# Kernel tuning notes

Hardware: AMD Instinct MI355X
Metric: run time of the kernel (lower is better)

The kernel has to match this reference:

```python
import jax, jax.numpy as jnp
import numpy as np

K = 1.0        # Lorentz manifold curvature parameter
EPS = 1e-7     # arccosh argument clamp (geoopt float32 eps)


def projx(x):
    # Project onto the hyperboloid: x0 = sqrt(K + ||x_1:||^2)
    rest = x[..., 1:]
    x0 = jnp.sqrt(K + jnp.sum(rest * rest, axis=-1, keepdims=True))
    return jnp.concatenate([x0, rest], axis=-1)


def setup_inputs() -> dict:
    key = jax.random.key(0)
    k1, k2 = jax.random.split(key)
    B, C, D = 16384, 2048, 512
    x = jax.random.normal(k1, (B, D), dtype=jnp.float32)
    # ManifoldParameter: random_normal with std = 1/sqrt(n_dim)
    points = jax.random.normal(k2, (C, D), dtype=jnp.float32) * (1.0 / np.sqrt(D))
    return {"x": x, "points": points}


def reference(x, points):
    xp = projx(x)        # (B, D) on hyperboloid
    pp = projx(points)   # (C, D) on hyperboloid
    # Minkowski inner <x,p>_L = -x0*p0 + sum_{i>0} x_i p_i = x.p - 2*x0*p0
    # Computed as a GEMM plus a rank-1 correction (avoids (B,C,D) intermediate).
    inner = xp @ pp.T - 2.0 * jnp.outer(xp[:, 0], pp[:, 0])  # (B, C)
    d = jnp.sqrt(K) * jnp.arccosh(jnp.maximum(-inner / K, 1.0 + EPS))
    return -d  # (B, C) negative Riemannian distances (class logits)
```

## Files before the change

### kernel.cpp

```cpp
#include <hip/hip_runtime.h>
#include <hip/hip_bf16.h>
#include <stdint.h>

#define B_ROWS 16384
#define C_ROWS 2048
#define D_FULL 512
#define KP     512

#define BM 128
#define BN 128
#define BK 64

typedef __attribute__((ext_vector_type(8))) short bf16x8;
typedef __attribute__((ext_vector_type(4))) float f32x4;

typedef __attribute__((address_space(1))) void glb_void;
typedef __attribute__((address_space(3))) void lds_void;

__device__ __forceinline__ void gld16(const void* g, void* l) {
    __builtin_amdgcn_global_load_lds((glb_void*)(uintptr_t)g,
                                     (lds_void*)(uintptr_t)l, 16, 0, 0);
}

__global__ __launch_bounds__(256) void prep_kernel(
    const float* __restrict__ x, const float* __restrict__ pts,
    unsigned short* __restrict__ Abf, unsigned short* __restrict__ Bbf,
    float* __restrict__ xn, float* __restrict__ pn)
{
    int row = blockIdx.x;
    const float* src;
    unsigned short* dst;
    float* nrm;
    if (row < B_ROWS) {
        src = x + (size_t)row * D_FULL;
        dst = Abf + (size_t)row * KP;
        nrm = xn + row;
    } else {
        int r = row - B_ROWS;
        src = pts + (size_t)r * D_FULL;
        dst = Bbf + (size_t)r * KP;
        nrm = pn + r;
    }
    int t = threadIdx.x;
    float v0 = src[2 * t + 1];
    float v1 = (t < 255) ? src[2 * t + 2] : 0.0f;
    __hip_bfloat16 b0 = __float2bfloat16(v0);
    __hip_bfloat16 b1 = __float2bfloat16(v1);
    union { unsigned short u[2]; unsigned int w; } pack;
    pack.u[0] = *(unsigned short*)&b0;
    pack.u[1] = *(unsigned short*)&b1;
    *(unsigned int*)&dst[2 * t] = pack.w;
    float ss = v0 * v0 + v1 * v1;
    #pragma unroll
    for (int off = 32; off > 0; off >>= 1) ss += __shfl_down(ss, off);
    __shared__ float red[4];
    if ((t & 63) == 0) red[t >> 6] = ss;
    __syncthreads();
    if (t == 0) nrm[0] = sqrtf(1.0f + red[0] + red[1] + red[2] + red[3]);
}

__global__ __launch_bounds__(256, 2) void gemm_kernel(
    const unsigned short* __restrict__ A,
    const unsigned short* __restrict__ Bm,
    const float* __restrict__ xn, const float* __restrict__ pn,
    float* __restrict__ out)
{
    __shared__ unsigned short As[2][BM * BK];
    __shared__ unsigned short Bs[2][BN * BK];

    const int tid  = threadIdx.x;
    const int wave = tid >> 6;
    const int lane = tid & 63;
    const int wm   = wave >> 1;
    const int wn   = wave & 1;
    const int lrow = lane & 15;
    const int quad = lane >> 4;

    const int bm0 = blockIdx.x * BM;
    const int bn0 = blockIdx.y * BN;

    const int srow = wave * 32 + (lane >> 3);
    const int scol = (((lane & 7) ^ ((lane >> 3) & 7)) << 3);

    const unsigned short* gA = A  + (size_t)(bm0 + srow) * KP + scol;
    const unsigned short* gB = Bm + (size_t)(bn0 + srow) * KP + scol;

    f32x4 acc[4][4] = {};

    #pragma unroll
    for (int i = 0; i < 4; ++i) {
        gld16(gA + (size_t)(i * 8) * KP, &As[0][(wave * 32 + i * 8) * BK]);
        gld16(gB + (size_t)(i * 8) * KP, &Bs[0][(wave * 32 + i * 8) * BK]);
    }

    #pragma unroll 2
    for (int it = 0; it < KP / BK; ++it) {
        const int buf = it & 1;
        __syncthreads();
        if (it + 1 < KP / BK) {
            const int k1 = (it + 1) * BK;
            #pragma unroll
            for (int i = 0; i < 4; ++i) {
                gld16(gA + (size_t)(i * 8) * KP + k1, &As[buf ^ 1][(wave * 32 + i * 8) * BK]);
                gld16(gB + (size_t)(i * 8) * KP + k1, &Bs[buf ^ 1][(wave * 32 + i * 8) * BK]);
            }
        }
        #pragma unroll
        for (int kk = 0; kk < BK; kk += 32) {
            const int ch0 = kk >> 3;
            bf16x8 af[4], bfr[4];
            #pragma unroll
            for (int mi = 0; mi < 4; ++mi) {
                int r = wm * 64 + mi * 16 + lrow;
                af[mi] = *(const bf16x8*)&As[buf][r * BK + (((ch0 + quad) ^ (lrow & 7)) << 3)];
            }
            #pragma unroll
            for (int ni = 0; ni < 4; ++ni) {
                int r = wn * 64 + ni * 16 + lrow;
                bfr[ni] = *(const bf16x8*)&Bs[buf][r * BK + (((ch0 + quad) ^ (lrow & 7)) << 3)];
            }
            #pragma unroll
            for (int mi = 0; mi < 4; ++mi)
                #pragma unroll
                for (int ni = 0; ni < 4; ++ni)
                    acc[mi][ni] = __builtin_amdgcn_mfma_f32_16x16x32_bf16(
                        af[mi], bfr[ni], acc[mi][ni], 0, 0, 0);
        }
    }

    float pv[4];
    #pragma unroll
    for (int ni = 0; ni < 4; ++ni)
        pv[ni] = pn[bn0 + wn * 64 + ni * 16 + lrow];

    #pragma unroll
    for (int mi = 0; mi < 4; ++mi) {
        #pragma unroll
        for (int r = 0; r < 4; ++r) {
            int row = bm0 + wm * 64 + mi * 16 + quad * 4 + r;
            float xv = xn[row];
            size_t base = (size_t)row * C_ROWS + bn0 + wn * 64 + lrow;
            #pragma unroll
            for (int ni = 0; ni < 4; ++ni) {
                float z = fmaf(xv, pv[ni], -acc[mi][ni][r]);
                z = fmaxf(z, 1.0f + 1e-7f);
                out[base + ni * 16] = -__logf(z + __fsqrt_rn(z * z - 1.0f));
            }
        }
    }
}

extern "C" void kernel_launch(void* const* d_in, const int* in_sizes, int n_in,
                              void* d_out, int out_size, void* d_ws, size_t ws_size,
                              hipStream_t stream) {
    const float* x   = (const float*)d_in[0];
    const float* pts = (const float*)d_in[1];
    float* out = (float*)d_out;

    char* ws = (char*)d_ws;
    unsigned short* Abf = (unsigned short*)ws;
    unsigned short* Bbf = (unsigned short*)(ws + (size_t)B_ROWS * KP * 2);
    float* xn = (float*)(ws + (size_t)(B_ROWS + C_ROWS) * KP * 2);
    float* pn = (float*)((char*)xn + (size_t)B_ROWS * 4);
    (void)in_sizes; (void)n_in; (void)out_size; (void)ws_size;

    prep_kernel<<<B_ROWS + C_ROWS, 256, 0, stream>>>(x, pts, Abf, Bbf, xn, pn);

    dim3 grid(B_ROWS / BM, C_ROWS / BN);
    gemm_kernel<<<grid, 256, 0, stream>>>(Abf, Bbf, xn, pn, out);
}
```

Measured before the change: 196.1 us.

## Restructure GEMM into persistent strip blocks streaming full-K A chunks with B from global

Replaces the 2D tiled GEMM grid with 256 persistent blocks, each owning a 128-column strip of points and a range of 1024 rows of x. Each block streams 64-row full-K chunks of A into double-buffered LDS and reads B fragments directly from global (relying on cache), running the epilogue per chunk. The aim is to cut B reloads through LDS and launch overhead and to overlap the A prefetch with the epilogue. It risks low occupancy (one block per CU, large LDS), B fragment loads that hit global memory every k-step, and only 256 blocks to fill the device.

```diff
diff --git a/kernel.cpp b/kernel.cpp
--- a/kernel.cpp
+++ b/kernel.cpp
@@ -7,9 +7,10 @@
 #define D_FULL 512
 #define KP     512
 
-#define BM 128
-#define BN 128
-#define BK 64
+#define STRIPS  16
+#define MSPLIT  16
+#define CHUNK_M 64
+#define NCHUNK  16
 
 typedef __attribute__((ext_vector_type(8))) short bf16x8;
 typedef __attribute__((ext_vector_type(4))) float f32x4;
@@ -59,14 +60,13 @@
     if (t == 0) nrm[0] = sqrtf(1.0f + red[0] + red[1] + red[2] + red[3]);
 }
 
-__global__ __launch_bounds__(256, 2) void gemm_kernel(
+__global__ __launch_bounds__(256, 1) void gemm_kernel(
     const unsigned short* __restrict__ A,
     const unsigned short* __restrict__ Bm,
     const float* __restrict__ xn, const float* __restrict__ pn,
     float* __restrict__ out)
 {
-    __shared__ unsigned short As[2][BM * BK];
-    __shared__ unsigned short Bs[2][BN * BK];
+    __shared__ unsigned short As[2][CHUNK_M * KP];
 
     const int tid  = threadIdx.x;
     const int wave = tid >> 6;
@@ -76,75 +76,82 @@
     const int lrow = lane & 15;
     const int quad = lane >> 4;
 
-    const int bm0 = blockIdx.x * BM;
-    const int bn0 = blockIdx.y * BN;
+    const int m     = blockIdx.x & 15;
+    const int s     = blockIdx.x >> 4;
+    const int n0    = s * 128;
+    const int mBase = m * (CHUNK_M * NCHUNK);
 
-    const int srow = wave * 32 + (lane >> 3);
-    const int scol = (((lane & 7) ^ ((lane >> 3) & 7)) << 3);
+    const unsigned short* bPtr[4];
+    #pragma unroll
+    for (int nt = 0; nt < 4; ++nt)
+        bPtr[nt] = Bm + (size_t)(n0 + wn * 64 + nt * 16 + lrow) * KP + quad * 8;
 
-    const unsigned short* gA = A  + (size_t)(bm0 + srow) * KP + scol;
-    const unsigned short* gB = Bm + (size_t)(bn0 + srow) * KP + scol;
+    const int colEven = (lane ^ wave) << 3;
+    const int colOdd  = (lane ^ (wave + 4)) << 3;
 
-    f32x4 acc[4][4] = {};
+    const unsigned short* gA = A + (size_t)(mBase)*KP;
 
-    #pragma unroll
-    for (int i = 0; i < 4; ++i) {
-        gld16(gA + (size_t)(i * 8) * KP, &As[0][(wave * 32 + i * 8) * BK]);
-        gld16(gB + (size_t)(i * 8) * KP, &Bs[0][(wave * 32 + i * 8) * BK]);
-    }
-
-    #pragma unroll 2
-    for (int it = 0; it < KP / BK; ++it) {
-        const int buf = it & 1;
-        __syncthreads();
-        if (it + 1 < KP / BK) {
-            const int k1 = (it + 1) * BK;
-            #pragma unroll
-            for (int i = 0; i < 4; ++i) {
-                gld16(gA + (size_t)(i * 8) * KP + k1, &As[buf ^ 1][(wave * 32 + i * 8) * BK]);
-                gld16(gB + (size_t)(i * 8) * KP + k1, &Bs[buf ^ 1][(wave * 32 + i * 8) * BK]);
-            }
-        }
-        #pragma unroll
-        for (int kk = 0; kk < BK; kk += 32) {
-            const int ch0 = kk >> 3;
-            bf16x8 af[4], bfr[4];
-            #pragma unroll
-            for (int mi = 0; mi < 4; ++mi) {
-                int r = wm * 64 + mi * 16 + lrow;
-                af[mi] = *(const bf16x8*)&As[buf][r * BK + (((ch0 + quad) ^ (lrow & 7)) << 3)];
-            }
-            #pragma unroll
-            for (int ni = 0; ni < 4; ++ni) {
-                int r = wn * 64 + ni * 16 + lrow;
-                bfr[ni] = *(const bf16x8*)&Bs[buf][r * BK + (((ch0 + quad) ^ (lrow & 7)) << 3)];
-            }
-            #pragma unroll
-            for (int mi = 0; mi < 4; ++mi)
-                #pragma unroll
-                for (int ni = 0; ni < 4; ++ni)
-                    acc[mi][ni] = __builtin_amdgcn_mfma_f32_16x16x32_bf16(
-                        af[mi], bfr[ni], acc[mi][ni], 0, 0, 0);
-        }
-    }
+    const int sA = lrow & 7;
 
     float pv[4];
     #pragma unroll
-    for (int ni = 0; ni < 4; ++ni)
-        pv[ni] = pn[bn0 + wn * 64 + ni * 16 + lrow];
+    for (int nt = 0; nt < 4; ++nt)
+        pv[nt] = pn[n0 + wn * 64 + nt * 16 + lrow];
 
     #pragma unroll
-    for (int mi = 0; mi < 4; ++mi) {
+    for (int i = 0; i < 16; ++i) {
+        int r = i * 4 + wave;
+        gld16(gA + (size_t)r * KP + ((i & 1) ? colOdd : colEven), &As[0][r * KP]);
+    }
+
+    for (int ch = 0; ch < NCHUNK; ++ch) {
+        const int buf = ch & 1;
+        __syncthreads();
+
+        f32x4 acc[2][4] = {};
         #pragma unroll
-        for (int r = 0; r < 4; ++r) {
-            int row = bm0 + wm * 64 + mi * 16 + quad * 4 + r;
-            float xv = xn[row];
-            size_t base = (size_t)row * C_ROWS + bn0 + wn * 64 + lrow;
+        for (int ks = 0; ks < 16; ++ks) {
+            bf16x8 af[2], bfr[4];
             #pragma unroll
-            for (int ni = 0; ni < 4; ++ni) {
-                float z = fmaf(xv, pv[ni], -acc[mi][ni][r]);
-                z = fmaxf(z, 1.0f + 1e-7f);
-                out[base + ni * 16] = -__logf(z + __fsqrt_rn(z * z - 1.0f));
+            for (int mt = 0; mt < 2; ++mt) {
+                int rl = wm * 32 + mt * 16 + lrow;
+                int chunk = ((ks * 4 + quad) ^ sA);
+                af[mt] = *(const bf16x8*)&As[buf][rl * KP + (chunk << 3)];
+            }
+            #pragma unroll
+            for (int nt = 0; nt < 4; ++nt)
+                bfr[nt] = *(const bf16x8*)(bPtr[nt] + ks * 32);
+            #pragma unroll
+            for (int mt = 0; mt < 2; ++mt)
+                #pragma unroll
+                for (int nt = 0; nt < 4; ++nt)
+                    acc[mt][nt] = __builtin_amdgcn_mfma_f32_16x16x32_bf16(
+                        af[mt], bfr[nt], acc[mt][nt], 0, 0, 0);
+        }
+
+        if (ch + 1 < NCHUNK) {
+            const unsigned short* gAn = gA + (size_t)(ch + 1) * CHUNK_M * KP;
+            #pragma unroll
+            for (int i = 0; i < 16; ++i) {
+                int r = i * 4 + wave;
+                gld16(gAn + (size_t)r * KP + ((i & 1) ? colOdd : colEven),
+                      &As[buf ^ 1][r * KP]);
+            }
+        }
+
+        #pragma unroll
+        for (int mt = 0; mt < 2; ++mt) {
+            #pragma unroll
+            for (int r = 0; r < 4; ++r) {
+                int row = mBase + ch * CHUNK_M + wm * 32 + mt * 16 + quad * 4 + r;
+                float xv = xn[row];
+                size_t base = (size_t)row * C_ROWS + n0 + wn * 64 + lrow;
+                #pragma unroll
+                for (int nt = 0; nt < 4; ++nt) {
+                    float z = fmaf(xv, pv[nt], -acc[mt][nt][r]);
+                    z = fmaxf(z, 1.0f + 1e-7f);
+                    out[base + nt * 16] = -__logf(z + __fsqrt_rn(z * z - 1.0f));
+                }
             }
         }
     }
@@ -166,6 +173,5 @@
 
     prep_kernel<<<B_ROWS + C_ROWS, 256, 0, stream>>>(x, pts, Abf, Bbf, xn, pn);
 
-    dim3 grid(B_ROWS / BM, C_ROWS / BN);
-    gemm_kernel<<<grid, 256, 0, stream>>>(Abf, Bbf, xn, pn, out);
+    gemm_kernel<<<STRIPS * MSPLIT, 256, 0, stream>>>(Abf, Bbf, xn, pn, out);
 }
```

Measured after the change: 230.2 us. +17.4%, slower.

## Load B fragments directly from global into registers, bypassing LDS

Applied to the files above, without the earlier changes.

The B operand is no longer staged through shared memory. Each wave instead loads its bf16 B fragments straight from global memory into registers, with a one-step register prefetch. This halves LDS usage and removes the LDS reads for B, at the cost of more VGPRs and duplicate global loads across the waves that share B rows. The launch-bounds occupancy hint of 2 is also dropped, and the K loop is no longer unrolled by 2.

```diff
diff --git a/kernel.cpp b/kernel.cpp
--- a/kernel.cpp
+++ b/kernel.cpp
@@ -59,14 +59,13 @@
     if (t == 0) nrm[0] = sqrtf(1.0f + red[0] + red[1] + red[2] + red[3]);
 }
 
-__global__ __launch_bounds__(256, 2) void gemm_kernel(
+__global__ __launch_bounds__(256) void gemm_kernel(
     const unsigned short* __restrict__ A,
     const unsigned short* __restrict__ Bm,
     const float* __restrict__ xn, const float* __restrict__ pn,
     float* __restrict__ out)
 {
     __shared__ unsigned short As[2][BM * BK];
-    __shared__ unsigned short Bs[2][BN * BK];
 
     const int tid  = threadIdx.x;
     const int wave = tid >> 6;
@@ -81,51 +80,62 @@
 
     const int srow = wave * 32 + (lane >> 3);
     const int scol = (((lane & 7) ^ ((lane >> 3) & 7)) << 3);
+    const unsigned short* gA = A + (size_t)(bm0 + srow) * KP + scol;
 
-    const unsigned short* gA = A  + (size_t)(bm0 + srow) * KP + scol;
-    const unsigned short* gB = Bm + (size_t)(bn0 + srow) * KP + scol;
+    const unsigned short* bPtr[4];
+    #pragma unroll
+    for (int nt = 0; nt < 4; ++nt)
+        bPtr[nt] = Bm + (size_t)(bn0 + wn * 64 + nt * 16 + lrow) * KP + quad * 8;
 
     f32x4 acc[4][4] = {};
 
     #pragma unroll
-    for (int i = 0; i < 4; ++i) {
+    for (int i = 0; i < 4; ++i)
         gld16(gA + (size_t)(i * 8) * KP, &As[0][(wave * 32 + i * 8) * BK]);
-        gld16(gB + (size_t)(i * 8) * KP, &Bs[0][(wave * 32 + i * 8) * BK]);
-    }
 
-    #pragma unroll 2
+    bf16x8 bcur[2][4], bnxt[2][4];
+    #pragma unroll
+    for (int h = 0; h < 2; ++h)
+        #pragma unroll
+        for (int nt = 0; nt < 4; ++nt)
+            bcur[h][nt] = *(const bf16x8*)(bPtr[nt] + h * 32);
+
     for (int it = 0; it < KP / BK; ++it) {
         const int buf = it & 1;
+        const int k1 = (it + 1) * BK;
         __syncthreads();
         if (it + 1 < KP / BK) {
-            const int k1 = (it + 1) * BK;
             #pragma unroll
-            for (int i = 0; i < 4; ++i) {
-                gld16(gA + (size_t)(i * 8) * KP + k1, &As[buf ^ 1][(wave * 32 + i * 8) * BK]);
-                gld16(gB + (size_t)(i * 8) * KP + k1, &Bs[buf ^ 1][(wave * 32 + i * 8) * BK]);
-            }
+            for (int i = 0; i < 4; ++i)
+                gld16(gA + (size_t)(i * 8) * KP + k1,
+                      &As[buf ^ 1][(wave * 32 + i * 8) * BK]);
+            #pragma unroll
+            for (int h = 0; h < 2; ++h)
+                #pragma unroll
+                for (int nt = 0; nt < 4; ++nt)
+                    bnxt[h][nt] = *(const bf16x8*)(bPtr[nt] + k1 + h * 32);
         }
         #pragma unroll
         for (int kk = 0; kk < BK; kk += 32) {
             const int ch0 = kk >> 3;
-            bf16x8 af[4], bfr[4];
+            bf16x8 af[4];
             #pragma unroll
             for (int mi = 0; mi < 4; ++mi) {
                 int r = wm * 64 + mi * 16 + lrow;
                 af[mi] = *(const bf16x8*)&As[buf][r * BK + (((ch0 + quad) ^ (lrow & 7)) << 3)];
             }
             #pragma unroll
-            for (int ni = 0; ni < 4; ++ni) {
-                int r = wn * 64 + ni * 16 + lrow;
-                bfr[ni] = *(const bf16x8*)&Bs[buf][r * BK + (((ch0 + quad) ^ (lrow & 7)) << 3)];
-            }
-            #pragma unroll
             for (int mi = 0; mi < 4; ++mi)
                 #pragma unroll
                 for (int ni = 0; ni < 4; ++ni)
                     acc[mi][ni] = __builtin_amdgcn_mfma_f32_16x16x32_bf16(
-                        af[mi], bfr[ni], acc[mi][ni], 0, 0, 0);
+                        af[mi], bcur[kk >> 5][ni], acc[mi][ni], 0, 0, 0);
         }
+        #pragma unroll
+        for (int h = 0; h < 2; ++h)
+            #pragma unroll
+            for (int nt = 0; nt < 4; ++nt)
+                bcur[h][nt] = bnxt[h][nt];
     }
 
     float pv[4];
```

Measured after the change: 228.1 us. +16.3%, slower.
